# Optimization experiments

Hardware: AMD Instinct MI355X
Metric: run time of the kernel (lower is better)

Reference implementation:

```python
import jax, jax.numpy as jnp
import numpy as np

D_MODEL = 1024
N_HEADS = 16
HEAD_DIM = D_MODEL // N_HEADS
WINDOW = 256


def setup_inputs() -> dict:
    key = jax.random.key(0)
    k1, k2, k3 = jax.random.split(key, 3)
    x = jax.random.normal(k1, (1, 4096, D_MODEL), dtype=jnp.float32)
    # torch nn.Linear weights: [out_features, in_features]
    W_qkv = jax.random.normal(k2, (3 * D_MODEL, D_MODEL), dtype=jnp.float32) * (D_MODEL ** -0.5)
    W_proj = jax.random.normal(k3, (D_MODEL, D_MODEL), dtype=jnp.float32) * (D_MODEL ** -0.5)
    return {"x": x, "W_qkv": W_qkv, "W_proj": W_proj}


def reference(x, W_qkv, W_proj):
    B, T, D = x.shape
    H, Hd = N_HEADS, HEAD_DIM
    qkv = (x @ W_qkv.T).reshape(B, T, 3, H, Hd)
    qkv = jnp.transpose(qkv, (2, 0, 3, 1, 4))  # [3, B, H, T, Hd]
    q, k, v = qkv[0], qkv[1], qkv[2]
    # causal + sliding-window mask: allowed iff 0 <= i - j < WINDOW
    i = jnp.arange(T)[:, None]
    j = jnp.arange(T)[None, :]
    mask = (j <= i) & (j >= i - (WINDOW - 1))  # [T, T] bool
    scale = Hd ** -0.5
    attn = jnp.einsum('bhid,bhjd->bhij', q, k) * scale
    attn = jnp.where(mask, attn, -jnp.inf)
    attn = jax.nn.softmax(attn, axis=-1)
    out = jnp.einsum('bhij,bhjd->bhid', attn, v)  # [B, H, T, Hd]
    out = jnp.transpose(out, (0, 2, 1, 3)).reshape(B, T, D)
    return out @ W_proj.T
```

## Files before the change

kernel.cpp:

```cpp
#include <hip/hip_runtime.h>
#include <hip/hip_bf16.h>


#define T_SEQ   4096
#define DM      1024
#define NH      16
#define HD      64
#define WIN     256

typedef unsigned short u16_t;
typedef u16_t  u16v8 __attribute__((ext_vector_type(8)));
typedef __bf16 bf16v8 __attribute__((ext_vector_type(8)));
typedef float  f32v4 __attribute__((ext_vector_type(4)));

__device__ __forceinline__ f32v4 mfma_bf16(u16v8 a, u16v8 b, f32v4 c) {
    return __builtin_amdgcn_mfma_f32_16x16x32_bf16(
        __builtin_bit_cast(bf16v8, a), __builtin_bit_cast(bf16v8, b), c, 0, 0, 0);
}

__device__ __forceinline__ u16_t f2bf(float f) {
    unsigned u = __builtin_bit_cast(unsigned, f);
    u += 0x7fffu + ((u >> 16) & 1u);
    return (u16_t)(u >> 16);
}

__device__ __forceinline__ void gload_lds16(const u16_t* g, u16_t* l) {
    __builtin_amdgcn_global_load_lds(
        (const __attribute__((address_space(1))) unsigned int*)g,
        (__attribute__((address_space(3))) unsigned int*)l, 16, 0, 0);
}

__global__ void cvt_kernel(const float* __restrict__ in, u16_t* __restrict__ out, int n8) {
    int i = blockIdx.x * blockDim.x + threadIdx.x;
    if (i >= n8) return;
    const float4* p = (const float4*)(in + (size_t)i * 8);
    float4 a = p[0], b = p[1];
    u16v8 o;
    o[0] = f2bf(a.x); o[1] = f2bf(a.y); o[2] = f2bf(a.z); o[3] = f2bf(a.w);
    o[4] = f2bf(b.x); o[5] = f2bf(b.y); o[6] = f2bf(b.z); o[7] = f2bf(b.w);
    *(u16v8*)(out + (size_t)i * 8) = o;
}

template <typename OutT>
__global__ __launch_bounds__(256) void gemm_bt(const u16_t* __restrict__ A,
                                               const u16_t* __restrict__ B,
                                               OutT* __restrict__ C,
                                               int M, int N, int K) {
    __shared__ u16_t lA[128 * 32];
    __shared__ u16_t lB[128 * 32];
    const int tid = threadIdx.x;
    const int l  = tid & 63;
    const int w  = tid >> 6;
    const int lr = l & 15, ko = l >> 4;
    const int wr = (w >> 1) * 64, wc = (w & 1) * 64;
    const int arow0 = blockIdx.y * 128, bcol0 = blockIdx.x * 128;

    f32v4 acc[4][4];
#pragma unroll
    for (int m = 0; m < 4; ++m)
#pragma unroll
        for (int n = 0; n < 4; ++n) acc[m][n] = f32v4{0.f, 0.f, 0.f, 0.f};

    const int s0 = tid, s1 = tid + 256;
    const int r0 = s0 >> 2, g0 = s0 & 3;
    const int r1 = s1 >> 2, g1 = s1 & 3;
    const int k0q = (g0 ^ ((r0 >> 1) & 3)) * 8;
    const int k1q = (g1 ^ ((r1 >> 1) & 3)) * 8;

    for (int kt = 0; kt < K; kt += 32) {
        __syncthreads();
        gload_lds16(A + (size_t)(arow0 + r0) * K + kt + k0q, lA + s0 * 8);
        gload_lds16(A + (size_t)(arow0 + r1) * K + kt + k1q, lA + s1 * 8);
        gload_lds16(B + (size_t)(bcol0 + r0) * K + kt + k0q, lB + s0 * 8);
        gload_lds16(B + (size_t)(bcol0 + r1) * K + kt + k1q, lB + s1 * 8);
        __syncthreads();

        u16v8 af[4], bfv[4];
#pragma unroll
        for (int m = 0; m < 4; ++m) {
            int row = wr + m * 16 + lr;
            af[m] = *(const u16v8*)(lA + row * 32 + (ko ^ ((row >> 1) & 3)) * 8);
        }
#pragma unroll
        for (int n = 0; n < 4; ++n) {
            int row = wc + n * 16 + lr;
            bfv[n] = *(const u16v8*)(lB + row * 32 + (ko ^ ((row >> 1) & 3)) * 8);
        }
#pragma unroll
        for (int m = 0; m < 4; ++m)
#pragma unroll
            for (int n = 0; n < 4; ++n)
                acc[m][n] = mfma_bf16(af[m], bfv[n], acc[m][n]);
    }

#pragma unroll
    for (int m = 0; m < 4; ++m) {
        int crow0 = arow0 + wr + m * 16 + ko * 4;
#pragma unroll
        for (int n = 0; n < 4; ++n) {
            int ccol = bcol0 + wc + n * 16 + lr;
#pragma unroll
            for (int j = 0; j < 4; ++j) {
                float v = acc[m][n][j];
                if constexpr (sizeof(OutT) == 2)
                    C[(size_t)(crow0 + j) * N + ccol] = (OutT)f2bf(v);
                else
                    C[(size_t)(crow0 + j) * N + ccol] = (OutT)v;
            }
        }
    }
}

__global__ __launch_bounds__(256) void vtrans_kernel(const u16_t* __restrict__ qkv,
                                                     u16_t* __restrict__ vt) {
    __shared__ u16_t tile[64][72];
    const int t0 = blockIdx.x * 64, h = blockIdx.y;
    const int tid = threadIdx.x;
    {
        int r = tid >> 2, c = (tid & 3) * 16;
        const u16_t* src = qkv + (size_t)(t0 + r) * (3 * DM) + 2 * DM + h * HD + c;
        *(u16v8*)&tile[r][c]     = *(const u16v8*)src;
        *(u16v8*)&tile[r][c + 8] = *(const u16v8*)(src + 8);
    }
    __syncthreads();
    {
        int d = tid >> 2, ts = (tid & 3) * 16;
        u16_t* dst = vt + ((size_t)h * HD + d) * T_SEQ + t0 + ts;
        u16v8 o0, o1;
#pragma unroll
        for (int i = 0; i < 8; ++i) { o0[i] = tile[ts + i][d]; o1[i] = tile[ts + 8 + i][d]; }
        *(u16v8*)dst       = o0;
        *(u16v8*)(dst + 8) = o1;
    }
}

__global__ __launch_bounds__(256) void attn_kernel(const u16_t* __restrict__ qkv,
                                                   const u16_t* __restrict__ vt,
                                                   u16_t* __restrict__ out) {
    __shared__ u16_t pbuf[4][16 * 32];
    const int h = blockIdx.y;
    const int w = threadIdx.x >> 6, l = threadIdx.x & 63;
    const int i0 = blockIdx.x * 64 + w * 16;
    const int lr = l & 15, g = l >> 4;
    u16_t* P = pbuf[w];

    const u16_t* qb = qkv + h * HD;
    const u16_t* kb = qkv + DM + h * HD;

    u16v8 qf0, qf1;
    {
        const u16_t* qrow = qb + (size_t)(i0 + lr) * (3 * DM) + g * 8;
        qf0 = *(const u16v8*)qrow;
        qf1 = *(const u16v8*)(qrow + 32);
    }
    f32v4 o[4];
#pragma unroll
    for (int n = 0; n < 4; ++n) o[n] = f32v4{0.f, 0.f, 0.f, 0.f};
    float m_run[4], l_run[4];
#pragma unroll
    for (int j = 0; j < 4; ++j) { m_run[j] = -1e30f; l_run[j] = 0.f; }

    const int clo = (i0 - (WIN - 1) > 0 ? i0 - (WIN - 1) : 0) & ~31;
    const int chi = (i0 + 15) & ~31;
    for (int c = clo; c <= chi; c += 32) {
        f32v4 s[2];
#pragma unroll
        for (int kt = 0; kt < 2; ++kt) {
            const u16_t* krow = kb + (size_t)(c + kt * 16 + lr) * (3 * DM) + g * 8;
            u16v8 kf0 = *(const u16v8*)krow;
            u16v8 kf1 = *(const u16v8*)(krow + 32);
            f32v4 z = f32v4{0.f, 0.f, 0.f, 0.f};
            z = mfma_bf16(qf0, kf0, z);
            z = mfma_bf16(qf1, kf1, z);
            s[kt] = z;
        }
        float mloc[4], corr[4], rsum[4];
#pragma unroll
        for (int j = 0; j < 4; ++j) {
            const int i = i0 + g * 4 + j;
#pragma unroll
            for (int kt = 0; kt < 2; ++kt) {
                const int jg = c + kt * 16 + lr;
                float v = s[kt][j] * 0.125f;
                const bool okm = (jg <= i) && (jg >= i - (WIN - 1));
                s[kt][j] = okm ? v : -3e38f;
            }
            mloc[j] = fmaxf(s[0][j], s[1][j]);
        }
#pragma unroll
        for (int d = 1; d < 16; d <<= 1)
#pragma unroll
            for (int j = 0; j < 4; ++j) mloc[j] = fmaxf(mloc[j], __shfl_xor(mloc[j], d, 64));
#pragma unroll
        for (int j = 0; j < 4; ++j) {
            float mnew = fmaxf(m_run[j], mloc[j]);
            corr[j] = __expf(m_run[j] - mnew);
            m_run[j] = mnew;
            float p0 = __expf(s[0][j] - mnew);
            float p1 = __expf(s[1][j] - mnew);
            P[(g * 4 + j) * 32 + lr]      = f2bf(p0);
            P[(g * 4 + j) * 32 + 16 + lr] = f2bf(p1);
            rsum[j] = p0 + p1;
        }
#pragma unroll
        for (int d = 1; d < 16; d <<= 1)
#pragma unroll
            for (int j = 0; j < 4; ++j) rsum[j] += __shfl_xor(rsum[j], d, 64);
#pragma unroll
        for (int j = 0; j < 4; ++j) l_run[j] = l_run[j] * corr[j] + rsum[j];
#pragma unroll
        for (int n = 0; n < 4; ++n)
#pragma unroll
            for (int j = 0; j < 4; ++j) o[n][j] *= corr[j];

        u16v8 pa = *(const u16v8*)(P + lr * 32 + g * 8);
#pragma unroll
        for (int n = 0; n < 4; ++n) {
            const u16_t* vrow = vt + ((size_t)h * HD + n * 16 + lr) * T_SEQ + c + g * 8;
            u16v8 vf = *(const u16v8*)vrow;
            o[n] = mfma_bf16(pa, vf, o[n]);
        }
    }
#pragma unroll
    for (int n = 0; n < 4; ++n)
#pragma unroll
        for (int j = 0; j < 4; ++j) {
            int t = i0 + g * 4 + j;
            out[(size_t)t * DM + h * HD + n * 16 + lr] = f2bf(o[n][j] / l_run[j]);
        }
}

extern "C" void kernel_launch(void* const* d_in, const int* in_sizes, int n_in,
                              void* d_out, int out_size, void* d_ws, size_t ws_size,
                              hipStream_t stream) {
    const float* x     = (const float*)d_in[0];
    const float* wqkv  = (const float*)d_in[1];
    const float* wproj = (const float*)d_in[2];
    float* out = (float*)d_out;
    char* ws = (char*)d_ws;

    u16_t* xb     = (u16_t*)(ws);
    u16_t* wqkvb  = (u16_t*)(ws + (size_t)(8u << 20));
    u16_t* wprojb = (u16_t*)(ws + (size_t)(14u << 20));
    u16_t* qkvb   = (u16_t*)(ws + (size_t)(16u << 20));
    u16_t* vt     = (u16_t*)(ws + (size_t)(40u << 20));
    u16_t* attnb  = (u16_t*)(ws);

    const int n8x = T_SEQ * DM / 8, n8q = 3 * DM * DM / 8, n8p = DM * DM / 8;
    cvt_kernel<<<(n8x + 255) / 256, 256, 0, stream>>>(x, xb, n8x);
    cvt_kernel<<<(n8q + 255) / 256, 256, 0, stream>>>(wqkv, wqkvb, n8q);
    cvt_kernel<<<(n8p + 255) / 256, 256, 0, stream>>>(wproj, wprojb, n8p);

    gemm_bt<u16_t><<<dim3(3 * DM / 128, T_SEQ / 128), 256, 0, stream>>>(
        xb, wqkvb, qkvb, T_SEQ, 3 * DM, DM);

    vtrans_kernel<<<dim3(T_SEQ / 64, NH), 256, 0, stream>>>(qkvb, vt);

    attn_kernel<<<dim3(T_SEQ / 64, NH), 256, 0, stream>>>(qkvb, vt, attnb);

    gemm_bt<float><<<dim3(DM / 128, T_SEQ / 128), 256, 0, stream>>>(
        attnb, wprojb, out, T_SEQ, DM, DM);
}
```

Before: 192.7 us.

## Stage K/V tiles in swizzled LDS with double buffering in attention kernel

The attention kernel now loads 64-key K and V chunks cooperatively into double-buffered, XOR-swizzled shared memory through global_load_lds, so all four waves share one copy instead of each wave reading K/V from global memory. Chunks widen from 32 to 64 keys. Fully unmasked chunks skip the per-element mask test, and the exponentials use exp2 with log2(e) folded into the scale. In exchange it adds a block-wide barrier per chunk and uses more LDS, which can reduce occupancy. Chunk start is now aligned per block, so some chunks are processed that are entirely masked for particular waves.

Measured after the change: 175.0 us. 9.2% less time.

```diff
diff --git a/kernel.cpp b/kernel.cpp
--- a/kernel.cpp
+++ b/kernel.cpp
@@ -22,6 +22,10 @@
     unsigned u = __builtin_bit_cast(unsigned, f);
     u += 0x7fffu + ((u >> 16) & 1u);
     return (u16_t)(u >> 16);
+}
+
+__device__ __forceinline__ float exp2_fast(float x) {
+    return __builtin_amdgcn_exp2f(x);
 }
 
 __device__ __forceinline__ void gload_lds16(const u16_t* g, u16_t* l) {
@@ -137,22 +141,30 @@
 __global__ __launch_bounds__(256) void attn_kernel(const u16_t* __restrict__ qkv,
                                                    const u16_t* __restrict__ vt,
                                                    u16_t* __restrict__ out) {
-    __shared__ u16_t pbuf[4][16 * 32];
+    __shared__ u16_t lK[2][64 * 64];
+    __shared__ u16_t lV[2][64 * 64];
+    __shared__ u16_t pbuf[4][16 * 64];
+
     const int h = blockIdx.y;
-    const int w = threadIdx.x >> 6, l = threadIdx.x & 63;
-    const int i0 = blockIdx.x * 64 + w * 16;
+    const int q0 = blockIdx.x * 64;
+    const int tid = threadIdx.x;
+    const int w = tid >> 6, l = tid & 63;
     const int lr = l & 15, g = l >> 4;
+    const int i0 = q0 + w * 16;
     u16_t* P = pbuf[w];
 
-    const u16_t* qb = qkv + h * HD;
-    const u16_t* kb = qkv + DM + h * HD;
+    const int r_st = tid >> 3;
+    const int c8l  = tid & 7;
+    const u16_t* kBase = qkv + DM + h * HD;
+    const u16_t* vBase = vt + (size_t)h * HD * T_SEQ;
 
     u16v8 qf0, qf1;
     {
-        const u16_t* qrow = qb + (size_t)(i0 + lr) * (3 * DM) + g * 8;
+        const u16_t* qrow = qkv + h * HD + (size_t)(i0 + lr) * (3 * DM) + g * 8;
         qf0 = *(const u16v8*)qrow;
         qf1 = *(const u16v8*)(qrow + 32);
     }
+
     f32v4 o[4];
 #pragma unroll
     for (int n = 0; n < 4; ++n) o[n] = f32v4{0.f, 0.f, 0.f, 0.f};
@@ -160,33 +172,71 @@
 #pragma unroll
     for (int j = 0; j < 4; ++j) { m_run[j] = -1e30f; l_run[j] = 0.f; }
 
-    const int clo = (i0 - (WIN - 1) > 0 ? i0 - (WIN - 1) : 0) & ~31;
-    const int chi = (i0 + 15) & ~31;
-    for (int c = clo; c <= chi; c += 32) {
-        f32v4 s[2];
-#pragma unroll
-        for (int kt = 0; kt < 2; ++kt) {
-            const u16_t* krow = kb + (size_t)(c + kt * 16 + lr) * (3 * DM) + g * 8;
-            u16v8 kf0 = *(const u16v8*)krow;
-            u16v8 kf1 = *(const u16v8*)(krow + 32);
+    const int c0 = (q0 >= WIN) ? q0 - WIN : 0;
+    const int nch = ((q0 - c0) >> 6) + 1;
+
+#define STAGE_KV(buf, cc)                                                              \
+    do {                                                                               \
+        _Pragma("unroll")                                                              \
+        for (int p = 0; p < 2; ++p) {                                                  \
+            int rr = r_st + p * 32;                                                    \
+            int cs = c8l ^ (rr & 7);                                                   \
+            gload_lds16(kBase + (size_t)(cc + rr) * (3 * DM) + cs * 8,                 \
+                        lK[buf] + (size_t)(rr * 64 + c8l * 8));                        \
+            gload_lds16(vBase + (size_t)rr * T_SEQ + (cc) + cs * 8,                    \
+                        lV[buf] + (size_t)(rr * 64 + c8l * 8));                        \
+        }                                                                              \
+    } while (0)
+
+    STAGE_KV(0, c0);
+
+    const float sc = 0.125f * 1.4426950408889634f;
+
+    for (int ci = 0; ci < nch; ++ci) {
+        const int c = c0 + (ci << 6);
+        const int cur = ci & 1;
+        __syncthreads();
+        if (ci + 1 < nch) STAGE_KV(cur ^ 1, c + 64);
+
+        const u16_t* K = lK[cur];
+        const u16_t* V = lV[cur];
+
+        f32v4 s[4];
+#pragma unroll
+        for (int kt = 0; kt < 4; ++kt) {
+            int krow = kt * 16 + lr;
+            u16v8 k0 = *(const u16v8*)(K + krow * 64 + ((g     ^ (krow & 7)) * 8));
+            u16v8 k1 = *(const u16v8*)(K + krow * 64 + (((4+g) ^ (krow & 7)) * 8));
             f32v4 z = f32v4{0.f, 0.f, 0.f, 0.f};
-            z = mfma_bf16(qf0, kf0, z);
-            z = mfma_bf16(qf1, kf1, z);
+            z = mfma_bf16(qf0, k0, z);
+            z = mfma_bf16(qf1, k1, z);
             s[kt] = z;
         }
+
+        const bool full = (c + 63 <= i0) && (c >= i0 - 240);
+        if (full) {
+#pragma unroll
+            for (int kt = 0; kt < 4; ++kt)
+#pragma unroll
+                for (int j = 0; j < 4; ++j) s[kt][j] *= sc;
+        } else {
+#pragma unroll
+            for (int j = 0; j < 4; ++j) {
+                const int i = i0 + g * 4 + j;
+#pragma unroll
+                for (int kt = 0; kt < 4; ++kt) {
+                    const int jg = c + kt * 16 + lr;
+                    float v = s[kt][j] * sc;
+                    const bool okm = (jg <= i) && (jg >= i - (WIN - 1));
+                    s[kt][j] = okm ? v : -3e38f;
+                }
+            }
+        }
+
         float mloc[4], corr[4], rsum[4];
 #pragma unroll
-        for (int j = 0; j < 4; ++j) {
-            const int i = i0 + g * 4 + j;
-#pragma unroll
-            for (int kt = 0; kt < 2; ++kt) {
-                const int jg = c + kt * 16 + lr;
-                float v = s[kt][j] * 0.125f;
-                const bool okm = (jg <= i) && (jg >= i - (WIN - 1));
-                s[kt][j] = okm ? v : -3e38f;
-            }
-            mloc[j] = fmaxf(s[0][j], s[1][j]);
-        }
+        for (int j = 0; j < 4; ++j)
+            mloc[j] = fmaxf(fmaxf(s[0][j], s[1][j]), fmaxf(s[2][j], s[3][j]));
 #pragma unroll
         for (int d = 1; d < 16; d <<= 1)
 #pragma unroll
@@ -194,14 +244,21 @@
 #pragma unroll
         for (int j = 0; j < 4; ++j) {
             float mnew = fmaxf(m_run[j], mloc[j]);
-            corr[j] = __expf(m_run[j] - mnew);
+            corr[j] = exp2_fast(m_run[j] - mnew);
             m_run[j] = mnew;
-            float p0 = __expf(s[0][j] - mnew);
-            float p1 = __expf(s[1][j] - mnew);
-            P[(g * 4 + j) * 32 + lr]      = f2bf(p0);
-            P[(g * 4 + j) * 32 + 16 + lr] = f2bf(p1);
-            rsum[j] = p0 + p1;
-        }
+            rsum[j] = 0.f;
+        }
+#pragma unroll
+        for (int kt = 0; kt < 4; ++kt)
+#pragma unroll
+            for (int j = 0; j < 4; ++j) {
+                float p = exp2_fast(s[kt][j] - m_run[j]);
+                rsum[j] += p;
+                int rP = g * 4 + j;
+                int col = kt * 16 + lr;
+                int c8 = col >> 3;
+                P[rP * 64 + ((c8 ^ (rP & 7)) * 8 + (col & 7))] = f2bf(p);
+            }
 #pragma unroll
         for (int d = 1; d < 16; d <<= 1)
 #pragma unroll
@@ -213,14 +270,19 @@
 #pragma unroll
             for (int j = 0; j < 4; ++j) o[n][j] *= corr[j];
 
-        u16v8 pa = *(const u16v8*)(P + lr * 32 + g * 8);
+        u16v8 pa0 = *(const u16v8*)(P + lr * 64 + ((g     ^ (lr & 7)) * 8));
+        u16v8 pa1 = *(const u16v8*)(P + lr * 64 + (((4+g) ^ (lr & 7)) * 8));
 #pragma unroll
         for (int n = 0; n < 4; ++n) {
-            const u16_t* vrow = vt + ((size_t)h * HD + n * 16 + lr) * T_SEQ + c + g * 8;
-            u16v8 vf = *(const u16v8*)vrow;
-            o[n] = mfma_bf16(pa, vf, o[n]);
-        }
-    }
+            int vrow = n * 16 + lr;
+            u16v8 v0 = *(const u16v8*)(V + vrow * 64 + ((g     ^ (vrow & 7)) * 8));
+            u16v8 v1 = *(const u16v8*)(V + vrow * 64 + (((4+g) ^ (vrow & 7)) * 8));
+            o[n] = mfma_bf16(pa0, v0, o[n]);
+            o[n] = mfma_bf16(pa1, v1, o[n]);
+        }
+    }
+#undef STAGE_KV
+
 #pragma unroll
     for (int n = 0; n < 4; ++n)
 #pragma unroll
```
